# Kernel optimization log

Measured on AMD Instinct MI355X. Metric: run time of the kernel, lower is better.

## Reference

```python
import jax, jax.numpy as jnp
import numpy as np

L, D = 1024, 256
NDIR, NL = 6, 2
H, P, N, K = 8, 64, 32, 4          # nheads, headdim, d_state, d_conv
DI = 2 * D                          # d_inner = expand * d_model
DIN = 2 * DI + 2 * N + H            # in_proj output width (z, xBC, dt)
CONV_DIM = DI + 2 * N               # channels going through depthwise conv
ORDERS = [(0, 1, 2), (0, 2, 1), (1, 0, 2), (1, 2, 0), (2, 0, 1), (2, 1, 0)]  # XYT,XTY,YXT,YTX,TXY,TYX


def setup_inputs() -> dict:
    ks = jax.random.split(jax.random.key(0), 12)
    s = 0.02
    f32 = jnp.float32
    return {
        "vectors": jax.random.normal(ks[0], (L, D), f32),
        "event_coords": jax.random.randint(ks[1], (L, 4), 0, 64, jnp.int32),
        "ln_g": jnp.ones((NDIR, NL, D), f32),
        "ln_b": jnp.zeros((NDIR, NL, D), f32),
        "Win": jax.random.normal(ks[2], (NDIR, NL, D, DIN), f32) * s,
        "conv_w": jax.random.normal(ks[3], (NDIR, NL, CONV_DIM, K), f32) * s,
        "conv_b": jnp.zeros((NDIR, NL, CONV_DIM), f32),
        "dt_bias": jax.random.normal(ks[4], (NDIR, NL, H), f32) * 0.5,
        "A_log": jnp.log(jax.random.uniform(ks[5], (NDIR, NL, H), f32, 1.0, 16.0)),
        "Dp": jnp.ones((NDIR, NL, H), f32),
        "rms_g": jnp.ones((NDIR, NL, DI), f32),
        "Wout": jax.random.normal(ks[6], (NDIR, NL, DI, D), f32) * s,
        "fuse_ln_g": jnp.ones((NDIR * D,), f32),
        "fuse_ln_b": jnp.zeros((NDIR * D,), f32),
        "fuse_W": jax.random.normal(ks[7], (NDIR * D, D), f32) * s,
        "fuse_b": jnp.zeros((D,), f32),
    }


def _layernorm(x, g, b, eps=1e-5):
    mu = jnp.mean(x, -1, keepdims=True)
    var = jnp.mean((x - mu) ** 2, -1, keepdims=True)
    return (x - mu) * jax.lax.rsqrt(var + eps) * g + b


def _causal_dwconv(x, w, b):
    # x: [Bt,L,C]; w: [C,K]. Torch depthwise conv1d with padding K-1, truncated to L.
    k = w.shape[1]
    Lx = x.shape[1]
    xp = jnp.pad(x, ((0, 0), (k - 1, 0), (0, 0)))
    return sum(xp[:, j:j + Lx, :] * w[:, j] for j in range(k)) + b


def _mamba2(x, Win, conv_w, conv_b, dt_bias, A_log, Dp, rms_g, Wout):
    # x: [Bt,L,D] -> [Bt,L,D]. Mamba2 with ngroups=1, rmsnorm gating, no proj biases.
    Bt, Lx, _ = x.shape
    zxbcdt = x @ Win
    z = zxbcdt[..., :DI]
    xBC = zxbcdt[..., DI:DI + CONV_DIM]
    dt = jax.nn.softplus(zxbcdt[..., -H:] + dt_bias)              # [Bt,L,H]
    xBC = jax.nn.silu(_causal_dwconv(xBC, conv_w, conv_b))
    xs = xBC[..., :DI].reshape(Bt, Lx, H, P)                      # [Bt,L,H,P]
    Bm = xBC[..., DI:DI + N]                                      # [Bt,L,N]
    Cm = xBC[..., DI + N:]                                        # [Bt,L,N]
    dA = jnp.exp(dt * (-jnp.exp(A_log)))                          # [Bt,L,H]
    dBx = jnp.einsum('blh,bln,blhp->blhpn', dt, Bm, xs)

    def step(h, inp):
        dA_t, dBx_t, C_t = inp
        h = dA_t[:, :, None, None] * h + dBx_t                    # [Bt,H,P,N]
        return h, jnp.einsum('bhpn,bn->bhp', h, C_t)

    h0 = jnp.zeros((Bt, H, P, N), x.dtype)
    _, ys = jax.lax.scan(step, h0, (dA.transpose(1, 0, 2),
                                    dBx.transpose(1, 0, 2, 3, 4),
                                    Cm.transpose(1, 0, 2)))
    y = ys.transpose(1, 0, 2, 3) + Dp[:, None] * xs               # [Bt,L,H,P]
    u = y.reshape(Bt, Lx, DI) * jax.nn.silu(z)                    # gated RMSNorm
    u = u * jax.lax.rsqrt(jnp.mean(u * u, -1, keepdims=True) + 1e-5) * rms_g
    return u @ Wout


def _forward(vectors, event_coords, ln_g, ln_b, Win, conv_w, conv_b, dt_bias,
             A_log, Dp, rms_g, Wout, fuse_ln_g, fuse_ln_b, fuse_W, fuse_b):
    v = vectors[None]                                             # [1,L,D]
    outs = []
    for i, axes in enumerate(ORDERS):
        idx = jnp.lexsort(tuple(event_coords[:, a] for a in reversed(axes)))
        x = v[:, idx, :]
        for l in range(NL):
            x = x + _mamba2(_layernorm(x, ln_g[i, l], ln_b[i, l]),
                            Win[i, l], conv_w[i, l], conv_b[i, l], dt_bias[i, l],
                            A_log[i, l], Dp[i, l], rms_g[i, l], Wout[i, l])
        outs.append(x[:, jnp.argsort(idx), :])                    # scatter back
    md = jnp.concatenate(outs, -1)                                # [1,L,6D]
    f = _layernorm(md, fuse_ln_g, fuse_ln_b) @ fuse_W + fuse_b
    return jax.nn.gelu(f, approximate=False)[0]                   # [L,D]


def reference(vectors, event_coords, ln_g, ln_b, Win, conv_w, conv_b, dt_bias,
              A_log, Dp, rms_g, Wout, fuse_ln_g, fuse_ln_b, fuse_W, fuse_b):
    return _forward(vectors, event_coords, ln_g, ln_b, Win, conv_w, conv_b, dt_bias,
                    A_log, Dp, rms_g, Wout, fuse_ln_g, fuse_ln_b, fuse_W, fuse_b)
```

## Files before the change

### kernel.cpp

```cpp
#include <hip/hip_runtime.h>
#include <hip/hip_bf16.h>
#include <cstddef>

#define LL 1024
#define DD0 256
#define NDIR 6
#define NL 2
#define HH 8
#define PP 64
#define NN 32
#define KK 4
#define DI 512
#define DIN 1096
#define CONV_DIM 576

#define QC 32
#define NC 32
#define NCSH 5

__constant__ int c_ord[6][3] = {{0,1,2},{0,2,1},{1,0,2},{1,2,0},{2,0,1},{2,1,0}};

typedef __attribute__((ext_vector_type(8))) short bf16x8;
typedef __attribute__((ext_vector_type(4))) float f32x4;

__device__ inline float blockReduceSum256(float v) {
    __shared__ float sred[4];
#pragma unroll
    for (int off = 1; off < 64; off <<= 1) v += __shfl_xor(v, off);
    int lane = threadIdx.x & 63, w = threadIdx.x >> 6;
    __syncthreads();
    if (lane == 0) sred[w] = v;
    __syncthreads();
    return sred[0] + sred[1] + sred[2] + sred[3];
}

__device__ inline float siluf(float x) { return x / (1.f + expf(-x)); }

__device__ inline unsigned short bf16_rn(float x) {
    unsigned u = __float_as_uint(x);
    unsigned r = (u + 0x7fffu + ((u >> 16) & 1u)) >> 16;
    return (unsigned short)r;
}
__device__ inline float bf16_to_f(unsigned short h) {
    return __uint_as_float(((unsigned)h) << 16);
}

__global__ __launch_bounds__(1024)
void sort_kernel(const int* __restrict__ coords, int* __restrict__ perm, int* __restrict__ rank) {
    int d = blockIdx.x;
    int i = threadIdx.x;
    __shared__ unsigned keys[LL];
    int a0 = c_ord[d][0], a1 = c_ord[d][1], a2 = c_ord[d][2];
    unsigned c0 = (unsigned)coords[i*4 + a0];
    unsigned c1 = (unsigned)coords[i*4 + a1];
    unsigned c2 = (unsigned)coords[i*4 + a2];
    unsigned key = (c0 << 22) | (c1 << 16) | (c2 << 10) | (unsigned)i;
    keys[i] = key;
    __syncthreads();
    int r = 0;
    for (int j = 0; j < LL; ++j) r += (keys[j] < key) ? 1 : 0;
    perm[d*LL + r] = i;
    rank[d*LL + i] = r;
}

__global__ __launch_bounds__(256)
void gather_ln(const float* __restrict__ vectors, const int* __restrict__ perm,
               float* __restrict__ x, unsigned short* __restrict__ Yh,
               unsigned short* __restrict__ Yl,
               const float* __restrict__ g, const float* __restrict__ b) {
    int t = blockIdx.x, d = blockIdx.y, c = threadIdx.x;
    int src = perm[d*LL + t];
    float xv = vectors[(size_t)src*DD0 + c];
    x[((size_t)d*LL + t)*DD0 + c] = xv;
    float s = blockReduceSum256(xv);
    float s2 = blockReduceSum256(xv*xv);
    float mu = s / DD0;
    float var = s2 / DD0 - mu*mu;
    float inv = rsqrtf(var + 1e-5f);
    const float* gr = g + (size_t)d*NL*DD0;
    const float* br = b + (size_t)d*NL*DD0;
    float yv = (xv - mu) * inv * gr[c] + br[c];
    unsigned short h = bf16_rn(yv);
    Yh[((size_t)d*LL + t)*DD0 + c] = h;
    Yl[((size_t)d*LL + t)*DD0 + c] = bf16_rn(yv - bf16_to_f(h));
}

__global__ __launch_bounds__(256)
void ln_split(const float* __restrict__ X, unsigned short* __restrict__ Yh,
              unsigned short* __restrict__ Yl,
              const float* __restrict__ g, const float* __restrict__ b,
              int dd, int rowsPerDir, int gstride) {
    int t = blockIdx.x, d = blockIdx.y;
    const float* xr = X + ((size_t)d*rowsPerDir + t)*dd;
    unsigned short* yh = Yh + ((size_t)d*rowsPerDir + t)*dd;
    unsigned short* yl = Yl + ((size_t)d*rowsPerDir + t)*dd;
    const float* gr = g + (size_t)d*gstride;
    const float* br = b + (size_t)d*gstride;
    float v[6];
    float s = 0.f, s2 = 0.f;
    int cnt = 0;
    for (int c = threadIdx.x; c < dd; c += 256) {
        float xv = xr[c];
        v[cnt++] = xv;
        s += xv; s2 += xv*xv;
    }
    float tot = blockReduceSum256(s);
    float tot2 = blockReduceSum256(s2);
    float mu = tot / dd;
    float var = tot2 / dd - mu*mu;
    float inv = rsqrtf(var + 1e-5f);
    cnt = 0;
    for (int c = threadIdx.x; c < dd; c += 256) {
        float yv = (v[cnt++] - mu) * inv * gr[c] + br[c];
        unsigned short h = bf16_rn(yv);
        yh[c] = h;
        yl[c] = bf16_rn(yv - bf16_to_f(h));
    }
}

__global__ __launch_bounds__(256)
void ln_concat(const float* __restrict__ x, const int* __restrict__ rank,
               unsigned short* __restrict__ Yh, unsigned short* __restrict__ Yl,
               const float* __restrict__ g, const float* __restrict__ b) {
    int t = blockIdx.x, tid = threadIdx.x;
    float v[NDIR];
    float s = 0.f, s2 = 0.f;
#pragma unroll
    for (int d = 0; d < NDIR; ++d) {
        int r = rank[d*LL + t];
        float xv = x[((size_t)d*LL + r)*DD0 + tid];
        v[d] = xv;
        s += xv; s2 += xv*xv;
    }
    float tot = blockReduceSum256(s);
    float tot2 = blockReduceSum256(s2);
    const int dd = NDIR*DD0;
    float mu = tot / dd;
    float var = tot2 / dd - mu*mu;
    float inv = rsqrtf(var + 1e-5f);
#pragma unroll
    for (int d = 0; d < NDIR; ++d) {
        int c = d*DD0 + tid;
        float yv = (v[d] - mu) * inv * g[c] + b[c];
        unsigned short h = bf16_rn(yv);
        Yh[(size_t)t*dd + c] = h;
        Yl[(size_t)t*dd + c] = bf16_rn(yv - bf16_to_f(h));
    }
}

__global__ __launch_bounds__(256)
void tsplit_kernel(const float* __restrict__ W, unsigned short* __restrict__ Th,
                   unsigned short* __restrict__ Tl, int Kd, int Nd) {
    __shared__ float tile[32][33];
    int j0 = blockIdx.x * 32;
    int i0 = blockIdx.y * 32;
    int c = threadIdx.x & 31, r8 = threadIdx.x >> 5;
    const float* Wz = W + (size_t)blockIdx.z * Kd * Nd;
    unsigned short* Thz = Th + (size_t)blockIdx.z * Nd * Kd;
    unsigned short* Tlz = Tl + (size_t)blockIdx.z * Nd * Kd;
#pragma unroll
    for (int s = 0; s < 4; ++s) {
        int i = i0 + r8 + s*8;
        tile[r8 + s*8][c] = (i < Kd && (j0 + c) < Nd) ? Wz[(size_t)i*Nd + j0 + c] : 0.f;
    }
    __syncthreads();
#pragma unroll
    for (int s = 0; s < 4; ++s) {
        int j = j0 + r8 + s*8;
        int i = i0 + c;
        if (j < Nd && i < Kd) {
            float xv = tile[c][r8 + s*8];
            unsigned short h = bf16_rn(xv);
            Thz[(size_t)j*Kd + i] = h;
            Tlz[(size_t)j*Kd + i] = bf16_rn(xv - bf16_to_f(h));
        }
    }
}

template<int MODE, int BM>
__global__ __launch_bounds__(256)
void mfma_gemm(const unsigned short* __restrict__ Ahg, const unsigned short* __restrict__ Alg,
               const unsigned short* __restrict__ Bhg, const unsigned short* __restrict__ Blg,
               float* __restrict__ Cg, int N, int K,
               size_t sA, size_t sB, size_t sC, const float* __restrict__ bias,
               int ksplit) {
    constexpr int MF = BM / 32;
    __shared__ unsigned short AhS[2][BM][40];
    __shared__ unsigned short AlS[2][BM][40];
    __shared__ unsigned short BhS[2][64][40];
    __shared__ unsigned short BlS[2][64][40];
    const unsigned short* Azh = Ahg + (MODE == 3 ? 0 : (size_t)blockIdx.z * sA);
    const unsigned short* Azl = Alg + (MODE == 3 ? 0 : (size_t)blockIdx.z * sA);
    const unsigned short* Bzh = Bhg + (MODE == 3 ? 0 : (size_t)blockIdx.z * sB);
    const unsigned short* Bzl = Blg + (MODE == 3 ? 0 : (size_t)blockIdx.z * sB);
    float* Cz = Cg + (size_t)blockIdx.z * sC;
    int row0 = blockIdx.y * BM;
    int col0 = blockIdx.x * 64;
    int tid = threadIdx.x;
    int lane = tid & 63, wid = tid >> 6;
    int mbase = (wid >> 1) * (BM/2), nbase = (wid & 1) * 32;
    int lr = lane & 15, lk = (lane >> 4) * 8;

    int ar0 = tid >> 2;
    int ar1 = 64 + (tid >> 2);
    int ac  = (tid & 3) * 8;
    int brow = tid >> 2;
    int bc8 = (tid & 3) * 8;
    bool bvalid = (col0 + brow) < N;
    const uint4 z4 = {0u,0u,0u,0u};

    f32x4 acc[MF][2];
#pragma unroll
    for (int m = 0; m < MF; ++m)
#pragma unroll
        for (int n = 0; n < 2; ++n) acc[m][n] = (f32x4){0.f, 0.f, 0.f, 0.f};

    uint4 s0a0, s0a1, s0l0, s0l1, s0bh, s0bl;
    uint4 s1a0, s1a1, s1l0, s1l1, s1bh, s1bl;

#define LOAD_TILE(Ra0,Ra1,Rl0,Rl1,Rbh,Rbl,kt) do {                          \
        size_t ka = (size_t)(kt) * 32;                                       \
        size_t g0 = (size_t)(row0 + ar0)*K + ka + ac;                        \
        Ra0 = *(const uint4*)(Azh + g0);                                     \
        Rl0 = *(const uint4*)(Azl + g0);                                     \
        if (BM == 128) {                                                     \
            size_t g1 = (size_t)(row0 + ar1)*K + ka + ac;                    \
            Ra1 = *(const uint4*)(Azh + g1);                                 \
            Rl1 = *(const uint4*)(Azl + g1);                                 \
        }                                                                    \
        if (bvalid) {                                                        \
            size_t gb = (size_t)(col0 + brow)*K + ka + bc8;                  \
            Rbh = *(const uint4*)(Bzh + gb);                                 \
            Rbl = *(const uint4*)(Bzl + gb);                                 \
        } else { Rbh = z4; Rbl = z4; }                                       \
    } while (0)

#define WRITE_TILE(buf,Ra0,Ra1,Rl0,Rl1,Rbh,Rbl) do {                         \
        *(uint4*)&AhS[buf][ar0][ac] = Ra0;                                   \
        *(uint4*)&AlS[buf][ar0][ac] = Rl0;                                   \
        if (BM == 128) {                                                     \
            *(uint4*)&AhS[buf][ar1 & (BM-1)][ac] = Ra1;                      \
            *(uint4*)&AlS[buf][ar1 & (BM-1)][ac] = Rl1;                      \
        }                                                                    \
        *(uint4*)&BhS[buf][brow][bc8] = Rbh;                                 \
        *(uint4*)&BlS[buf][brow][bc8] = Rbl;                                 \
    } while (0)

#define COMPUTE(buf) do {                                                    \
        bf16x8 afh[MF], afl[MF], bfh[2], bfl[2];                             \
        _Pragma("unroll")                                                    \
        for (int mf = 0; mf < MF; ++mf) {                                    \
            afh[mf] = *(const bf16x8*)&AhS[buf][mbase + mf*16 + lr][lk];     \
            afl[mf] = *(const bf16x8*)&AlS[buf][mbase + mf*16 + lr][lk];     \
        }                                                                    \
        _Pragma("unroll")                                                    \
        for (int nf = 0; nf < 2; ++nf) {                                     \
            bfh[nf] = *(const bf16x8*)&BhS[buf][nbase + nf*16 + lr][lk];     \
            bfl[nf] = *(const bf16x8*)&BlS[buf][nbase + nf*16 + lr][lk];     \
        }                                                                    \
        _Pragma("unroll")                                                    \
        for (int mf = 0; mf < MF; ++mf)                                      \
            _Pragma("unroll")                                                \
            for (int nf = 0; nf < 2; ++nf) {                                 \
                acc[mf][nf] = __builtin_amdgcn_mfma_f32_16x16x32_bf16(afh[mf], bfh[nf], acc[mf][nf], 0, 0, 0); \
                acc[mf][nf] = __builtin_amdgcn_mfma_f32_16x16x32_bf16(afh[mf], bfl[nf], acc[mf][nf], 0, 0, 0); \
                acc[mf][nf] = __builtin_amdgcn_mfma_f32_16x16x32_bf16(afl[mf], bfh[nf], acc[mf][nf], 0, 0, 0); \
            }                                                                \
    } while (0)

    int nt, kt0;
    if (MODE == 3) { nt = ksplit; kt0 = (int)blockIdx.z * ksplit; }
    else           { nt = K >> 5; kt0 = 0; }

    LOAD_TILE(s0a0, s0a1, s0l0, s0l1, s0bh, s0bl, kt0 + 0);
    LOAD_TILE(s1a0, s1a1, s1l0, s1l1, s1bh, s1bl, kt0 + 1);
    WRITE_TILE(0, s0a0, s0a1, s0l0, s0l1, s0bh, s0bl);
    __syncthreads();

    for (int t = 0; t < nt; t += 2) {
        if (t + 2 < nt) LOAD_TILE(s0a0, s0a1, s0l0, s0l1, s0bh, s0bl, kt0 + t + 2);
        COMPUTE(0);
        WRITE_TILE(1, s1a0, s1a1, s1l0, s1l1, s1bh, s1bl);
        __syncthreads();
        if (t + 3 < nt) LOAD_TILE(s1a0, s1a1, s1l0, s1l1, s1bh, s1bl, kt0 + t + 3);
        COMPUTE(1);
        if (t + 2 < nt) WRITE_TILE(0, s0a0, s0a1, s0l0, s0l1, s0bh, s0bl);
        __syncthreads();
    }

#undef LOAD_TILE
#undef WRITE_TILE
#undef COMPUTE

    int crb = (lane >> 4) * 4;
    int cco = lane & 15;
#pragma unroll
    for (int mf = 0; mf < MF; ++mf) {
#pragma unroll
        for (int nf = 0; nf < 2; ++nf) {
            int col = col0 + nbase + nf*16 + cco;
            if (col < N) {
#pragma unroll
                for (int r = 0; r < 4; ++r) {
                    int row = row0 + mbase + mf*16 + crb + r;
                    size_t o = (size_t)row*N + col;
                    float vv = acc[mf][nf][r];
                    if (MODE == 0 || MODE == 3) Cz[o] = vv;
                    else if (MODE == 1) Cz[o] += vv;
                    else {
                        vv += bias[col];
                        Cz[o] = 0.5f * vv * (1.f + erff(vv * 0.70710678118654752f));
                    }
                }
            }
        }
    }
}

__global__ __launch_bounds__(256)
void reduce_gelu(const float* __restrict__ pbuf, const float* __restrict__ bias,
                 float* __restrict__ out) {
    int t = blockIdx.x, c = threadIdx.x;
    size_t o = (size_t)t*DD0 + c;
    const size_t st = (size_t)LL*DD0;
    float v = pbuf[o] + pbuf[o + st] + pbuf[o + 2*st] + pbuf[o + 3*st] + bias[c];
    out[o] = 0.5f * v * (1.f + erff(v * 0.70710678118654752f));
}

__global__ __launch_bounds__(256)
void conv_scan1(const float* __restrict__ zx, const float* __restrict__ conv_w,
                const float* __restrict__ conv_b, const float* __restrict__ dt_bias,
                const float* __restrict__ A_log, const float* __restrict__ Dp,
                float* __restrict__ ys, float* __restrict__ Cbuf,
                float* __restrict__ cstate, float* __restrict__ cumdec, int layer) {
    int bid = blockIdx.x;
    int c = bid & (NC - 1);
    int hd = bid >> NCSH;
    int d = hd >> 3, h = hd & 7;
    int tid = threadIdx.x;
    int t0 = c * QC;

    __shared__ float sxc[QC][132];
    __shared__ float sdt[QC];
    __shared__ float sdA[QC];

    const float* Z = zx + (size_t)d*LL*DIN;

    {
        int col = tid & 127;
        int half = tid >> 7;
        int tstart = t0 + half*16;
        int realc = (col < 64) ? (h*PP + col) : ((col < 96) ? (DI + (col-64)) : (DI + NN + (col-96)));
        int zxcol = DI + realc;
        const float* wr = conv_w + ((size_t)(d*NL + layer)*CONV_DIM + realc)*KK;
        float w0 = wr[0], w1 = wr[1], w2 = wr[2], w3 = wr[3];
        float bias = conv_b[(size_t)(d*NL + layer)*CONV_DIM + realc];
        float z0 = (tstart-3 >= 0) ? Z[(size_t)(tstart-3)*DIN + zxcol] : 0.f;
        float z1 = (tstart-2 >= 0) ? Z[(size_t)(tstart-2)*DIN + zxcol] : 0.f;
        float z2 = (tstart-1 >= 0) ? Z[(size_t)(tstart-1)*DIN + zxcol] : 0.f;
#pragma unroll
        for (int tt = 0; tt < 16; ++tt) {
            int t = tstart + tt;
            float z3 = Z[(size_t)t*DIN + zxcol];
            float acc = bias;
            acc = fmaf(z0, w0, acc);
            acc = fmaf(z1, w1, acc);
            acc = fmaf(z2, w2, acc);
            acc = fmaf(z3, w3, acc);
            sxc[half*16 + tt][col] = siluf(acc);
            z0 = z1; z1 = z2; z2 = z3;
        }
    }
    if (tid < QC) {
        int t = t0 + tid;
        float v = Z[(size_t)t*DIN + (DIN - HH) + h] + dt_bias[(d*NL + layer)*HH + h];
        float sp = (v > 20.f) ? v : log1pf(expf(v));
        sdt[tid] = sp;
        sdA[tid] = expf(-expf(A_log[(d*NL + layer)*HH + h]) * sp);
    }
    __syncthreads();

    int p = tid >> 2, g = tid & 3, n0 = g << 3;
    float dpv = Dp[(d*NL + layer)*HH + h];
    float* ysd = ys + (size_t)d*LL*DI + h*PP + p;
    float* cdd = cumdec + (size_t)d*LL*HH + h;
    float* Cbd = Cbuf + (size_t)d*LL*NN;

    float hs[8];
#pragma unroll
    for (int j = 0; j < 8; ++j) hs[j] = 0.f;
    float cum = 1.f;

    for (int tt = 0; tt < QC; ++tt) {
        float dtv = sdt[tt], dAv = sdA[tt];
        float xv = sxc[tt][p];
        float dtx = dtv * xv;
        float4 b0 = *(const float4*)&sxc[tt][64 + n0];
        float4 b1 = *(const float4*)&sxc[tt][64 + n0 + 4];
        float4 c0 = *(const float4*)&sxc[tt][96 + n0];
        float4 c1 = *(const float4*)&sxc[tt][96 + n0 + 4];
        float B[8] = {b0.x,b0.y,b0.z,b0.w,b1.x,b1.y,b1.z,b1.w};
        float Cv[8] = {c0.x,c0.y,c0.z,c0.w,c1.x,c1.y,c1.z,c1.w};
        float acc = 0.f;
#pragma unroll
        for (int j = 0; j < 8; ++j) {
            hs[j] = fmaf(dAv, hs[j], dtx * B[j]);
            acc = fmaf(hs[j], Cv[j], acc);
        }
        acc += __shfl_xor(acc, 1);
        acc += __shfl_xor(acc, 2);
        int t = t0 + tt;
        if (g == 0) ysd[(size_t)t*DI] = acc + dpv * xv;
        else if (g == 2 && h == 0 && p < NN) Cbd[(size_t)t*NN + p] = sxc[tt][96 + p];
        cum *= dAv;
        if (tid == 0) cdd[(size_t)t*HH] = cum;
    }

    float* cs = cstate + (((size_t)(d*NC + c)*HH + h)*PP + p)*NN + n0;
    float4 s0 = {hs[0], hs[1], hs[2], hs[3]};
    float4 s1 = {hs[4], hs[5], hs[6], hs[7]};
    *(float4*)cs = s0;
    *(float4*)(cs + 4) = s1;
}

__global__ __launch_bounds__(256)
void scan_pass2(float* __restrict__ cstate, const float* __restrict__ cumdec) {
    int hd = blockIdx.x;
    int d = hd >> 3, h = hd & 7;
    int tid = threadIdx.x;
    int p = tid >> 2, g = tid & 3, n0 = g << 3;
    float carry[8];
#pragma unroll
    for (int j = 0; j < 8; ++j) carry[j] = 0.f;
    for (int c = 0; c < NC; ++c) {
        float* cs = cstate + (((size_t)(d*NC + c)*HH + h)*PP + p)*NN + n0;
        float4 s0 = *(const float4*)cs;
        float4 s1 = *(const float4*)(cs + 4);
        float4 w0 = {carry[0], carry[1], carry[2], carry[3]};
        float4 w1 = {carry[4], carry[5], carry[6], carry[7]};
        *(float4*)cs = w0;
        *(float4*)(cs + 4) = w1;
        float dec = cumdec[((size_t)d*LL + (c*QC + QC - 1))*HH + h];
        float s[8] = {s0.x,s0.y,s0.z,s0.w,s1.x,s1.y,s1.z,s1.w};
#pragma unroll
        for (int j = 0; j < 8; ++j) carry[j] = fmaf(dec, carry[j], s[j]);
    }
}

__global__ __launch_bounds__(256)
void scan_pass3(const float* __restrict__ Cbuf, const float* __restrict__ cumdec,
                const float* __restrict__ cstate, float* __restrict__ ys) {
    int bid = blockIdx.x;
    int c = bid & (NC - 1);
    if (c == 0) return;
    int hd = bid >> NCSH;
    int d = hd >> 3, h = hd & 7;
    int tid = threadIdx.x;
    int p = tid >> 2, g = tid & 3, n0 = g << 3;
    int t0 = c * QC;

    __shared__ float scd[QC];
    if (tid < QC) scd[tid] = cumdec[((size_t)d*LL + t0 + tid)*HH + h];

    const float* cs = cstate + (((size_t)(d*NC + c)*HH + h)*PP + p)*NN + n0;
    float4 h0 = *(const float4*)cs;
    float4 h1 = *(const float4*)(cs + 4);
    float hi[8] = {h0.x,h0.y,h0.z,h0.w,h1.x,h1.y,h1.z,h1.w};
    __syncthreads();

    const float* Cbd = Cbuf + (size_t)d*LL*NN;
    float* ysd = ys + (size_t)d*LL*DI + h*PP + p;

    for (int tt = 0; tt < QC; ++tt) {
        int t = t0 + tt;
        const float* row = Cbd + (size_t)t*NN;
        float4 c0 = *(const float4*)(row + n0);
        float4 c1 = *(const float4*)(row + n0 + 4);
        float Cv[8] = {c0.x,c0.y,c0.z,c0.w,c1.x,c1.y,c1.z,c1.w};
        float acc = 0.f;
#pragma unroll
        for (int j = 0; j < 8; ++j) acc = fmaf(hi[j], Cv[j], acc);
        acc += __shfl_xor(acc, 1);
        acc += __shfl_xor(acc, 2);
        if (g == 0) ysd[(size_t)t*DI] += scd[tt] * acc;
    }
}

__global__ __launch_bounds__(256)
void gate_rms(const float* __restrict__ ys, const float* __restrict__ zx,
              const float* __restrict__ rms_g, unsigned short* __restrict__ uh,
              unsigned short* __restrict__ ul, int layer) {
    int t = blockIdx.x, d = blockIdx.y;
    const float* ysr = ys + ((size_t)d*LL + t)*DI;
    const float* zr = zx + ((size_t)d*LL + t)*DIN;
    const float* rg = rms_g + (size_t)(d*NL + layer)*DI;
    unsigned short* uhr = uh + ((size_t)d*LL + t)*DI;
    unsigned short* ulr = ul + ((size_t)d*LL + t)*DI;
    int c2 = threadIdx.x * 2;
    float2 yv = *(const float2*)(ysr + c2);
    float2 zv = *(const float2*)(zr + c2);
    float u0 = yv.x * siluf(zv.x);
    float u1 = yv.y * siluf(zv.y);
    float ss = u0*u0 + u1*u1;
    float tot = blockReduceSum256(ss);
    float scale = rsqrtf(tot / DI + 1e-5f);
    float2 rgv = *(const float2*)(rg + c2);
    float o0 = u0 * scale * rgv.x;
    float o1 = u1 * scale * rgv.y;
    unsigned short h0 = bf16_rn(o0), h1 = bf16_rn(o1);
    unsigned short l0 = bf16_rn(o0 - bf16_to_f(h0)), l1 = bf16_rn(o1 - bf16_to_f(h1));
    *(unsigned*)(uhr + c2) = (unsigned)h0 | ((unsigned)h1 << 16);
    *(unsigned*)(ulr + c2) = (unsigned)l0 | ((unsigned)l1 << 16);
}

extern "C" void kernel_launch(void* const* d_in, const int* in_sizes, int n_in,
                              void* d_out, int out_size, void* d_ws, size_t ws_size,
                              hipStream_t stream) {
    const float* vectors   = (const float*)d_in[0];
    const int*   coords    = (const int*)d_in[1];
    const float* ln_g      = (const float*)d_in[2];
    const float* ln_b      = (const float*)d_in[3];
    const float* Win       = (const float*)d_in[4];
    const float* conv_w    = (const float*)d_in[5];
    const float* conv_b    = (const float*)d_in[6];
    const float* dt_bias   = (const float*)d_in[7];
    const float* A_log     = (const float*)d_in[8];
    const float* Dp        = (const float*)d_in[9];
    const float* rms_g     = (const float*)d_in[10];
    const float* Wout      = (const float*)d_in[11];
    const float* fuse_ln_g = (const float*)d_in[12];
    const float* fuse_ln_b = (const float*)d_in[13];
    const float* fuse_W    = (const float*)d_in[14];
    const float* fuse_b    = (const float*)d_in[15];
    float* out = (float*)d_out;

    char* ws = (char*)d_ws;
    size_t off = 0;
    auto alloc = [&](size_t bytes) -> void* {
        void* p = ws + off;
        off += (bytes + 255) & ~(size_t)255;
        return p;
    };
    int* perm  = (int*)alloc((size_t)NDIR*LL*4);
    int* rank  = (int*)alloc((size_t)NDIR*LL*4);
    float* x   = (float*)alloc((size_t)NDIR*LL*DD0*4);
    unsigned short* xnh = (unsigned short*)alloc((size_t)NDIR*LL*DD0*2);
    unsigned short* xnl = (unsigned short*)alloc((size_t)NDIR*LL*DD0*2);
    float* zx  = (float*)alloc((size_t)NDIR*LL*DIN*4);
    float* Cbuf= (float*)alloc((size_t)NDIR*LL*NN*4);
    float* ysb = (float*)alloc((size_t)NDIR*LL*DI*4);
    unsigned short* uh = (unsigned short*)alloc((size_t)NDIR*LL*DI*2);
    unsigned short* ul = (unsigned short*)alloc((size_t)NDIR*LL*DI*2);
    float* cstate = (float*)alloc((size_t)NDIR*NC*HH*PP*NN*4);
    float* cumdec = (float*)alloc((size_t)NDIR*LL*HH*4);
    float* pbuf  = (float*)alloc((size_t)4*LL*DD0*4);
    unsigned short* WinTh  = (unsigned short*)alloc((size_t)NDIR*NL*DIN*DD0*2);
    unsigned short* WinTl  = (unsigned short*)alloc((size_t)NDIR*NL*DIN*DD0*2);
    unsigned short* WoutTh = (unsigned short*)alloc((size_t)NDIR*NL*DD0*DI*2);
    unsigned short* WoutTl = (unsigned short*)alloc((size_t)NDIR*NL*DD0*DI*2);
    unsigned short* fWTh   = (unsigned short*)alloc((size_t)DD0*(NDIR*DD0)*2);
    unsigned short* fWTl   = (unsigned short*)alloc((size_t)DD0*(NDIR*DD0)*2);
    unsigned short* mdnh = uh;
    unsigned short* mdnl = ul;
    (void)ws_size;

    sort_kernel<<<NDIR, 1024, 0, stream>>>(coords, perm, rank);

    tsplit_kernel<<<dim3((DIN+31)/32, DD0/32, NDIR*NL), 256, 0, stream>>>(Win, WinTh, WinTl, DD0, DIN);
    tsplit_kernel<<<dim3(DD0/32, DI/32, NDIR*NL), 256, 0, stream>>>(Wout, WoutTh, WoutTl, DI, DD0);
    tsplit_kernel<<<dim3(DD0/32, (NDIR*DD0)/32, 1), 256, 0, stream>>>(fuse_W, fWTh, fWTl, NDIR*DD0, DD0);

    for (int l = 0; l < NL; ++l) {
        if (l == 0)
            gather_ln<<<dim3(LL, NDIR), 256, 0, stream>>>(vectors, perm, x, xnh, xnl, ln_g, ln_b);
        else
            ln_split<<<dim3(LL, NDIR), 256, 0, stream>>>(x, xnh, xnl, ln_g + l*DD0, ln_b + l*DD0,
                                                         DD0, LL, NL*DD0);
        mfma_gemm<0,64><<<dim3((DIN+63)/64, LL/64, NDIR), 256, 0, stream>>>(
            xnh, xnl, WinTh + (size_t)l*DIN*DD0, WinTl + (size_t)l*DIN*DD0, zx,
            DIN, DD0, (size_t)LL*DD0, (size_t)NL*DIN*DD0, (size_t)LL*DIN, nullptr, 0);
        conv_scan1<<<NDIR*HH*NC, 256, 0, stream>>>(zx, conv_w, conv_b, dt_bias, A_log, Dp,
                                                   ysb, Cbuf, cstate, cumdec, l);
        scan_pass2<<<NDIR*HH, 256, 0, stream>>>(cstate, cumdec);
        scan_pass3<<<NDIR*HH*NC, 256, 0, stream>>>(Cbuf, cumdec, cstate, ysb);
        gate_rms<<<dim3(LL, NDIR), 256, 0, stream>>>(ysb, zx, rms_g, uh, ul, l);
        mfma_gemm<1,64><<<dim3(DD0/64, LL/64, NDIR), 256, 0, stream>>>(
            uh, ul, WoutTh + (size_t)l*DD0*DI, WoutTl + (size_t)l*DD0*DI, x,
            DD0, DI, (size_t)LL*DI, (size_t)NL*DD0*DI, (size_t)LL*DD0, nullptr, 0);
    }

    ln_concat<<<LL, 256, 0, stream>>>(x, rank, mdnh, mdnl, fuse_ln_g, fuse_ln_b);
    mfma_gemm<3,64><<<dim3(DD0/64, LL/64, 4), 256, 0, stream>>>(
        mdnh, mdnl, fWTh, fWTl, pbuf, DD0, NDIR*DD0, 0, 0, (size_t)LL*DD0, nullptr, 12);
    reduce_gelu<<<LL, 256, 0, stream>>>(pbuf, fuse_b, out);
}
```

Measured before the change: 286.3 us.

## Fuse chunk-state carry, state output, and gated RMSNorm into one kernel; parallelize sort

Removes the serial inter-chunk carry kernel. Each block of the new fused kernel recomputes its incoming state from all previous chunk states, then applies the C·state correction, SiLU gating and RMSNorm with bf16 hi/lo split. This cuts two launches and the ys/cstate read-modify-write round trips. The cost is redundant prefix work that grows with chunk index, 64 state registers per thread, and only 192 blocks with a block reduction per timestep. The sort kernel is also split across 4 blocks per direction, with each thread counting over a quarter of the keys.

After: 386.0 us. 34.8% more time.

```diff
diff --git a/kernel.cpp b/kernel.cpp
--- a/kernel.cpp
+++ b/kernel.cpp
@@ -47,20 +47,33 @@
 
 __global__ __launch_bounds__(1024)
 void sort_kernel(const int* __restrict__ coords, int* __restrict__ perm, int* __restrict__ rank) {
-    int d = blockIdx.x;
-    int i = threadIdx.x;
+    int q = blockIdx.x, d = blockIdx.y;
+    int tid = threadIdx.x;
     __shared__ unsigned keys[LL];
+    __shared__ unsigned short part[256][5];
     int a0 = c_ord[d][0], a1 = c_ord[d][1], a2 = c_ord[d][2];
-    unsigned c0 = (unsigned)coords[i*4 + a0];
-    unsigned c1 = (unsigned)coords[i*4 + a1];
-    unsigned c2 = (unsigned)coords[i*4 + a2];
-    unsigned key = (c0 << 22) | (c1 << 16) | (c2 << 10) | (unsigned)i;
-    keys[i] = key;
-    __syncthreads();
+    {
+        unsigned c0 = (unsigned)coords[tid*4 + a0];
+        unsigned c1 = (unsigned)coords[tid*4 + a1];
+        unsigned c2 = (unsigned)coords[tid*4 + a2];
+        keys[tid] = (c0 << 22) | (c1 << 16) | (c2 << 10) | (unsigned)tid;
+    }
+    __syncthreads();
+    int il = tid >> 2, jq = tid & 3;
+    int i = q*256 + il;
+    unsigned ki = keys[i];
     int r = 0;
-    for (int j = 0; j < LL; ++j) r += (keys[j] < key) ? 1 : 0;
-    perm[d*LL + r] = i;
-    rank[d*LL + i] = r;
+    int j0 = jq*256;
+#pragma unroll 8
+    for (int j = j0; j < j0 + 256; ++j) r += (keys[j] < ki) ? 1 : 0;
+    part[il][jq] = (unsigned short)r;
+    __syncthreads();
+    if (tid < 256) {
+        int i2 = q*256 + tid;
+        int rr = part[tid][0] + part[tid][1] + part[tid][2] + part[tid][3];
+        perm[d*LL + rr] = i2;
+        rank[d*LL + i2] = rr;
+    }
 }
 
 __global__ __launch_bounds__(256)
@@ -424,93 +437,85 @@
 }
 
 __global__ __launch_bounds__(256)
-void scan_pass2(float* __restrict__ cstate, const float* __restrict__ cumdec) {
-    int hd = blockIdx.x;
-    int d = hd >> 3, h = hd & 7;
-    int tid = threadIdx.x;
-    int p = tid >> 2, g = tid & 3, n0 = g << 3;
-    float carry[8];
-#pragma unroll
-    for (int j = 0; j < 8; ++j) carry[j] = 0.f;
-    for (int c = 0; c < NC; ++c) {
-        float* cs = cstate + (((size_t)(d*NC + c)*HH + h)*PP + p)*NN + n0;
-        float4 s0 = *(const float4*)cs;
-        float4 s1 = *(const float4*)(cs + 4);
-        float4 w0 = {carry[0], carry[1], carry[2], carry[3]};
-        float4 w1 = {carry[4], carry[5], carry[6], carry[7]};
-        *(float4*)cs = w0;
-        *(float4*)(cs + 4) = w1;
-        float dec = cumdec[((size_t)d*LL + (c*QC + QC - 1))*HH + h];
-        float s[8] = {s0.x,s0.y,s0.z,s0.w,s1.x,s1.y,s1.z,s1.w};
-#pragma unroll
-        for (int j = 0; j < 8; ++j) carry[j] = fmaf(dec, carry[j], s[j]);
-    }
-}
-
-__global__ __launch_bounds__(256)
-void scan_pass3(const float* __restrict__ Cbuf, const float* __restrict__ cumdec,
-                const float* __restrict__ cstate, float* __restrict__ ys) {
+void pass3_gate(const float* __restrict__ ys, const float* __restrict__ zx,
+                const float* __restrict__ Cbuf, const float* __restrict__ cumdec,
+                const float* __restrict__ cstate, const float* __restrict__ rms_g,
+                unsigned short* __restrict__ uh, unsigned short* __restrict__ ul,
+                int layer) {
     int bid = blockIdx.x;
     int c = bid & (NC - 1);
-    if (c == 0) return;
-    int hd = bid >> NCSH;
-    int d = hd >> 3, h = hd & 7;
+    int d = bid >> NCSH;
     int tid = threadIdx.x;
-    int p = tid >> 2, g = tid & 3, n0 = g << 3;
     int t0 = c * QC;
-
-    __shared__ float scd[QC];
-    if (tid < QC) scd[tid] = cumdec[((size_t)d*LL + t0 + tid)*HH + h];
-
-    const float* cs = cstate + (((size_t)(d*NC + c)*HH + h)*PP + p)*NN + n0;
-    float4 h0 = *(const float4*)cs;
-    float4 h1 = *(const float4*)(cs + 4);
-    float hi[8] = {h0.x,h0.y,h0.z,h0.w,h1.x,h1.y,h1.z,h1.w};
-    __syncthreads();
-
+    int c0 = tid * 2;
+    int h0 = c0 >> 6;
+    int p0 = c0 & 63;
+
+    __shared__ float sC[NN];
+    __shared__ float sdc[QC][8];
+
+    {
+        int tt = tid >> 3, hh = tid & 7;
+        sdc[tt][hh] = cumdec[((size_t)d*LL + t0 + tt)*HH + hh];
+    }
+
+    float hi0[NN], hi1[NN];
+#pragma unroll
+    for (int j = 0; j < NN; ++j) { hi0[j] = 0.f; hi1[j] = 0.f; }
+    for (int j = 0; j < c; ++j) {
+        float dec = cumdec[((size_t)d*LL + (j*QC + QC - 1))*HH + h0];
+        const float* s0 = cstate + (((size_t)(d*NC + j)*HH + h0)*PP + p0)*NN;
+#pragma unroll
+        for (int jj = 0; jj < NN; jj += 4) {
+            float4 a = *(const float4*)(s0 + jj);
+            float4 b = *(const float4*)(s0 + NN + jj);
+            hi0[jj+0] = fmaf(dec, hi0[jj+0], a.x);
+            hi0[jj+1] = fmaf(dec, hi0[jj+1], a.y);
+            hi0[jj+2] = fmaf(dec, hi0[jj+2], a.z);
+            hi0[jj+3] = fmaf(dec, hi0[jj+3], a.w);
+            hi1[jj+0] = fmaf(dec, hi1[jj+0], b.x);
+            hi1[jj+1] = fmaf(dec, hi1[jj+1], b.y);
+            hi1[jj+2] = fmaf(dec, hi1[jj+2], b.z);
+            hi1[jj+3] = fmaf(dec, hi1[jj+3], b.w);
+        }
+    }
+
+    const float* ysd = ys + (size_t)d*LL*DI;
+    const float* zxd = zx + (size_t)d*LL*DIN;
     const float* Cbd = Cbuf + (size_t)d*LL*NN;
-    float* ysd = ys + (size_t)d*LL*DI + h*PP + p;
+    const float* rg = rms_g + (size_t)(d*NL + layer)*DI;
+    float2 rgv = *(const float2*)(rg + c0);
+    unsigned short* uhd = uh + (size_t)d*LL*DI;
+    unsigned short* uld = ul + (size_t)d*LL*DI;
+    __syncthreads();
 
     for (int tt = 0; tt < QC; ++tt) {
         int t = t0 + tt;
-        const float* row = Cbd + (size_t)t*NN;
-        float4 c0 = *(const float4*)(row + n0);
-        float4 c1 = *(const float4*)(row + n0 + 4);
-        float Cv[8] = {c0.x,c0.y,c0.z,c0.w,c1.x,c1.y,c1.z,c1.w};
-        float acc = 0.f;
-#pragma unroll
-        for (int j = 0; j < 8; ++j) acc = fmaf(hi[j], Cv[j], acc);
-        acc += __shfl_xor(acc, 1);
-        acc += __shfl_xor(acc, 2);
-        if (g == 0) ysd[(size_t)t*DI] += scd[tt] * acc;
-    }
-}
-
-__global__ __launch_bounds__(256)
-void gate_rms(const float* __restrict__ ys, const float* __restrict__ zx,
-              const float* __restrict__ rms_g, unsigned short* __restrict__ uh,
-              unsigned short* __restrict__ ul, int layer) {
-    int t = blockIdx.x, d = blockIdx.y;
-    const float* ysr = ys + ((size_t)d*LL + t)*DI;
-    const float* zr = zx + ((size_t)d*LL + t)*DIN;
-    const float* rg = rms_g + (size_t)(d*NL + layer)*DI;
-    unsigned short* uhr = uh + ((size_t)d*LL + t)*DI;
-    unsigned short* ulr = ul + ((size_t)d*LL + t)*DI;
-    int c2 = threadIdx.x * 2;
-    float2 yv = *(const float2*)(ysr + c2);
-    float2 zv = *(const float2*)(zr + c2);
-    float u0 = yv.x * siluf(zv.x);
-    float u1 = yv.y * siluf(zv.y);
-    float ss = u0*u0 + u1*u1;
-    float tot = blockReduceSum256(ss);
-    float scale = rsqrtf(tot / DI + 1e-5f);
-    float2 rgv = *(const float2*)(rg + c2);
-    float o0 = u0 * scale * rgv.x;
-    float o1 = u1 * scale * rgv.y;
-    unsigned short h0 = bf16_rn(o0), h1 = bf16_rn(o1);
-    unsigned short l0 = bf16_rn(o0 - bf16_to_f(h0)), l1 = bf16_rn(o1 - bf16_to_f(h1));
-    *(unsigned*)(uhr + c2) = (unsigned)h0 | ((unsigned)h1 << 16);
-    *(unsigned*)(ulr + c2) = (unsigned)l0 | ((unsigned)l1 << 16);
+        if (tid < NN) sC[tid] = Cbd[(size_t)t*NN + tid];
+        __syncthreads();
+        float dot0 = 0.f, dot1 = 0.f;
+#pragma unroll
+        for (int j = 0; j < NN; ++j) {
+            dot0 = fmaf(hi0[j], sC[j], dot0);
+            dot1 = fmaf(hi1[j], sC[j], dot1);
+        }
+        float cd = sdc[tt][h0];
+        float2 yv = *(const float2*)(ysd + (size_t)t*DI + c0);
+        float y0 = fmaf(cd, dot0, yv.x);
+        float y1 = fmaf(cd, dot1, yv.y);
+        float2 zv = *(const float2*)(zxd + (size_t)t*DIN + c0);
+        float u0 = y0 * siluf(zv.x);
+        float u1 = y1 * siluf(zv.y);
+        float tot = blockReduceSum256(u0*u0 + u1*u1);
+        float scale = rsqrtf(tot / DI + 1e-5f);
+        float o0 = u0 * scale * rgv.x;
+        float o1 = u1 * scale * rgv.y;
+        unsigned short hh0 = bf16_rn(o0), hh1 = bf16_rn(o1);
+        unsigned short ll0 = bf16_rn(o0 - bf16_to_f(hh0));
+        unsigned short ll1 = bf16_rn(o1 - bf16_to_f(hh1));
+        *(unsigned*)(uhd + (size_t)t*DI + c0) = (unsigned)hh0 | ((unsigned)hh1 << 16);
+        *(unsigned*)(uld + (size_t)t*DI + c0) = (unsigned)ll0 | ((unsigned)ll1 << 16);
+    }
 }
 
 extern "C" void kernel_launch(void* const* d_in, const int* in_sizes, int n_in,
@@ -564,7 +569,7 @@
     unsigned short* mdnl = ul;
     (void)ws_size;
 
-    sort_kernel<<<NDIR, 1024, 0, stream>>>(coords, perm, rank);
+    sort_kernel<<<dim3(4, NDIR), 1024, 0, stream>>>(coords, perm, rank);
 
     tsplit_kernel<<<dim3((DIN+31)/32, DD0/32, NDIR*NL), 256, 0, stream>>>(Win, WinTh, WinTl, DD0, DIN);
     tsplit_kernel<<<dim3(DD0/32, DI/32, NDIR*NL), 256, 0, stream>>>(Wout, WoutTh, WoutTl, DI, DD0);
@@ -581,9 +586,8 @@
             DIN, DD0, (size_t)LL*DD0, (size_t)NL*DIN*DD0, (size_t)LL*DIN, nullptr, 0);
         conv_scan1<<<NDIR*HH*NC, 256, 0, stream>>>(zx, conv_w, conv_b, dt_bias, A_log, Dp,
                                                    ysb, Cbuf, cstate, cumdec, l);
-        scan_pass2<<<NDIR*HH, 256, 0, stream>>>(cstate, cumdec);
-        scan_pass3<<<NDIR*HH*NC, 256, 0, stream>>>(Cbuf, cumdec, cstate, ysb);
-        gate_rms<<<dim3(LL, NDIR), 256, 0, stream>>>(ysb, zx, rms_g, uh, ul, l);
+        pass3_gate<<<NDIR*NC, 256, 0, stream>>>(ysb, zx, Cbuf, cumdec, cstate, rms_g,
+                                                uh, ul, l);
         mfma_gemm<1,64><<<dim3(DD0/64, LL/64, NDIR), 256, 0, stream>>>(
             uh, ul, WoutTh + (size_t)l*DD0*DI, WoutTl + (size_t)l*DD0*DI, x,
             DD0, DI, (size_t)LL*DI, (size_t)NL*DD0*DI, (size_t)LL*DD0, nullptr, 0);
```
